# Kernel tuning notes

Measured on AMD Instinct MI355X. Metric: run time of the kernel, lower is better.

## Reference

```python
import jax, jax.numpy as jnp
import numpy as np

LS = 64                      # latent_scaling
TYPES = [8, 1, 1]            # Pyr, SST, VIP widths
DEPTHS = [1, 1, 1]           # L4, L23, L5
B, T = 64, 256
I = 2 * 1 * len(TYPES) * len(DEPTHS)          # 18
AREA = sum(TYPES) * sum(DEPTHS) * LS          # 1920 per area
H = 2 * AREA                                  # 3840


def _build_mask():
    """Block-structured Bernoulli sign mask over 2 areas x (3 layers x 3 types).

    Mirrors the BB* buffers of celltypeRNN: within-area blocks drawn
    Bernoulli(p) with sign +1 for Pyr sources, -1 for SST/VIP sources;
    cross-area blocks zero.
    """
    rng = np.random.default_rng(0)
    # population order per area: (L4,Pyr),(L4,SST),(L4,VIP),(L23,...),(L5,...)
    sizes = [DEPTHS[l] * TYPES[t] * LS for l in range(3) for t in range(3)]
    offs = np.concatenate([[0], np.cumsum(sizes)])
    n_pop = 9
    # connection probability table P[src, dst] (from the source's pvals;
    # unspecified pairs default to 0.05)
    P = np.full((n_pop, n_pop), 0.05)
    # self blocks (diagonal): L4 [.1,.01,.03], L23 [.06,.05,.01], L5 [.04,.03,.03]
    diag = [0.10, 0.01, 0.03, 0.06, 0.05, 0.01, 0.04, 0.03, 0.03]
    for i, p in enumerate(diag):
        P[i, i] = p
    # L4Pyr (idx 0) -> others
    for dst, p in [(1, .04), (4, .04), (7, .03), (2, .00), (5, .02), (8, .11), (3, .07), (6, .00)]:
        P[0, dst] = p
    # L4SST (idx 1) -> others
    for dst, p in [(0, .22), (3, .33), (6, .08), (2, .22), (5, .21), (8, .07), (4, .05), (7, .04)]:
        P[1, dst] = p
    # L4VIP (idx 2) -> Pyr
    P[2, 0] = 0.0
    P[2, 3] = 0.0
    sign = np.array([+1.0, -1.0, -1.0] * 3)  # Pyr +, SST -, VIP -
    mask = np.zeros((H, H), dtype=np.float32)
    for area in range(2):           # V1, LM (within-area connectivity only)
        base = area * AREA
        for s in range(n_pop):
            for d in range(n_pop):
                r0, r1 = base + offs[d], base + offs[d + 1]
                c0, c1 = base + offs[s], base + offs[s + 1]
                blk = (rng.random((r1 - r0, c1 - c0)) < P[s, d]).astype(np.float32)
                mask[r0:r1, c0:c1] = blk * sign[s]
    return jnp.asarray(mask)


def setup_inputs() -> dict:
    key = jax.random.key(0)
    kx, kwi, kbi, kwh, kbh = jax.random.split(key, 5)
    s = 1.0 / np.sqrt(H)
    return {
        "x": jax.random.normal(kx, (B, T, I), jnp.float32),
        "W_ih": jax.random.uniform(kwi, (H, I), jnp.float32, -s, s),
        "b_ih": jax.random.uniform(kbi, (H,), jnp.float32, -s, s),
        "W_hh": jax.random.uniform(kwh, (H, H), jnp.float32, -s, s),
        "b_hh": jax.random.uniform(kbh, (H,), jnp.float32, -s, s),
        "mask": _build_mask(),
    }


def reference(x, W_ih, b_ih, W_hh, b_hh, mask):
    # cell-type connectivity mask applied to the recurrent weights
    Wm = W_hh * mask                              # [H, H]
    # precompute input projection for all timesteps: [B, T, H]
    xp = jnp.einsum("bti,hi->bth", x, W_ih) + b_ih + b_hh
    h0 = jnp.zeros((x.shape[0], Wm.shape[0]), x.dtype)

    def step(h, xp_t):                            # h: [B, H], xp_t: [B, H]
        h = jax.nn.relu(xp_t + h @ Wm.T)
        return h, h

    _, hs = jax.lax.scan(step, h0, jnp.swapaxes(xp, 0, 1))  # [T, B, H]
    return jnp.swapaxes(hs, 0, 1)                            # [B, T, H]
```

## Files before the change

### kernel.cpp

```cpp
#include <hip/hip_runtime.h>
#include <stdint.h>
#include <stddef.h>

#define HH 3840
#define AH 1920
#define NI 18
#define NT 256
#define NBATCH 64
#define KMAX 224
#define JSLOT 28
#define NRW 120
#define NB 8
#define NGROUP 16
#define NBLK_G 16
#define NBLOCKS 256
#define NTHREADS 1024
#define COLS 1920
#define COLT 1938
#define HNEW_PAD 9

#define ENT_BYTES ((size_t)HH * KMAX * 4)
#define CNT_BYTES ((size_t)HH * 4)
#define XT2_BYTES ((size_t)NT * NI * NBATCH * 2)
#define HT_HALF   ((size_t)NGROUP * AH * NB)
#define HT_BYTES  (2 * HT_HALF * 2)
#define FLAG_ELEMS ((size_t)NGROUP * NBLK_G * 32)
#define PC_ELEMS  16
#define PERM_BYTES ((size_t)HH * 4)

#define SLAB_B    (COLT * 16)
#define OFF_HNEW  (2 * SLAB_B)
#define HNEW_B    (2 * NRW * HNEW_PAD * 4)
#define OFF_IPERM (OFF_HNEW + HNEW_B)
#define SMEM_USED (OFF_IPERM + NRW * 4)
#define SMEM_ALLOC 83968

#define AS1 __attribute__((address_space(1)))
#define AS3 __attribute__((address_space(3)))

typedef unsigned long long u64;

__device__ __forceinline__ float lo16(uint32_t u) {
    union { uint16_t q; _Float16 h; } c; c.q = (uint16_t)u; return (float)c.h;
}
__device__ __forceinline__ uint16_t f2h_bits(float f) {
    union { _Float16 h; uint16_t u; } c; c.h = (_Float16)f; return c.u;
}
__device__ __forceinline__ uint32_t pkrtz(float x, float y) {
    typedef __fp16 h2 __attribute__((ext_vector_type(2)));
    union { h2 h; uint32_t u; } c; c.h = __builtin_amdgcn_cvt_pkrtz(x, y); return c.u;
}
__device__ __forceinline__ void gll16(const void* g, void* l) {
    __builtin_amdgcn_global_load_lds((const AS1 uint32_t*)g, (AS3 uint32_t*)l, 16, 0, 0);
}
__device__ __forceinline__ void astore(u64* p, u64 v) {
    __hip_atomic_store(p, v, __ATOMIC_RELAXED, __HIP_MEMORY_SCOPE_AGENT);
}
__device__ __forceinline__ uint32_t sel8(const uint32_t v[8], int b) {
    uint32_t x = v[0];
    #pragma unroll
    for (int i = 1; i < 8; ++i) x = (b == i) ? v[i] : x;
    return x;
}
__device__ __forceinline__ u64 sel8_64(const u64 v[8], int b) {
    u64 x = v[0];
    #pragma unroll
    for (int i = 1; i < 8; ++i) x = (b == i) ? v[i] : x;
    return x;
}
#define SWZ(v, pat) __uint_as_float(__builtin_amdgcn_ds_swizzle(__float_as_uint(v), pat))
#define DPA(c, ctrl) c += __uint_as_float(__builtin_amdgcn_mov_dpp(__float_as_uint(c), ctrl, 0xF, 0xF, true))
#define FMIX_LO(acc, h2, w) asm("v_fma_mix_f32 %0, %1, %2, %0 op_sel:[0,0,0] op_sel_hi:[1,0,0]" : "+v"(acc) : "v"(h2), "v"(w))
#define FMIX_HI(acc, h2, w) asm("v_fma_mix_f32 %0, %1, %2, %0 op_sel:[1,0,0] op_sel_hi:[1,0,0]" : "+v"(acc) : "v"(h2), "v"(w))

__global__ void init_ws_kernel(uint32_t* __restrict__ flg, uint32_t* __restrict__ ht0) {
    size_t i = (size_t)blockIdx.x * blockDim.x + threadIdx.x;
    if (i < FLAG_ELEMS + PC_ELEMS) flg[i] = 0;
    if (i < HT_HALF / 2) ht0[i] = 0;
}

__global__ void deg_kernel(const float* __restrict__ mask, uint32_t* __restrict__ deg) {
    int gw = (int)((blockIdx.x * blockDim.x + threadIdx.x) >> 6);
    int lane = threadIdx.x & 63;
    if (gw >= HH) return;
    int area = (gw >= AH) ? 1 : 0;
    const float* mrow = mask + (size_t)gw * HH + (size_t)area * AH;
    uint32_t n = 0;
    for (int c0 = 0; c0 < AH; c0 += 64)
        n += (uint32_t)__popcll(__ballot(mrow[c0 + lane] != 0.0f));
    if (lane == 0) deg[gw] = n + NI;
}

__global__ void perm_kernel(const uint32_t* __restrict__ deg,
                            uint32_t* __restrict__ posA, uint32_t* __restrict__ invA) {
    int d = blockIdx.x * blockDim.x + threadIdx.x;
    if (d >= HH) return;
    int area = (d >= AH) ? 1 : 0;
    int i = d - area * AH;
    const uint32_t* db = deg + (size_t)area * AH;
    uint32_t di = db[i];
    uint32_t rank = 0;
    for (int j = 0; j < AH; ++j) {
        uint32_t dj = db[j];
        rank += (dj > di || (dj == di && j < i)) ? 1u : 0u;
    }
    uint32_t chunk = rank >> 3, o = rank & 7;
    uint32_t pos = (chunk & 15) * NRW + (chunk >> 4) * 8 + o;
    posA[d] = pos;
    invA[(size_t)area * AH + pos] = (uint32_t)i;
}

__global__ void build_ell_kernel(const float* __restrict__ Whh, const float* __restrict__ mask,
                                 const float* __restrict__ Wih,
                                 const uint32_t* __restrict__ posA, const uint32_t* __restrict__ invA,
                                 uint32_t* __restrict__ ent, uint32_t* __restrict__ cnt) {
    int gw = (int)((blockIdx.x * blockDim.x + threadIdx.x) >> 6);
    int lane = threadIdx.x & 63;
    if (gw >= HH) return;
    const int area = (gw >= AH) ? 1 : 0;
    const int ol = (int)invA[gw];
    const size_t og = (size_t)area * AH + ol;
    const float* mrow = mask + og * HH + (size_t)area * AH;
    const float* wrow = Whh + og * HH + (size_t)area * AH;
    const uint32_t* pA = posA + (size_t)area * AH;
    uint32_t* erow = ent + (size_t)gw * KMAX;
    const u64 below = ((u64)1 << lane) - 1;

    uint32_t sz[8] = {0, 0, 0, 0, 0, 0, 0, 0};
    for (int c0 = 0; c0 <= AH; c0 += 64) {
        bool isx = (c0 == AH);
        bool pred; int b;
        if (isx) { pred = (lane < NI); b = lane & 7; }
        else     { pred = (mrow[c0 + lane] != 0.0f); b = (int)(pA[c0 + lane] & 7); }
        #pragma unroll
        for (int bb = 0; bb < 8; ++bb)
            sz[bb] += (uint32_t)__popcll(__ballot(pred && (b == bb)));
    }
    uint32_t run[8] = {0, 0, 0, 0, 0, 0, 0, 0};
    for (int c0 = 0; c0 <= AH; c0 += 64) {
        bool isx = (c0 == AH);
        int col; bool pred; float wval; int b;
        if (isx) {
            col = COLS + lane; pred = (lane < NI); b = lane & 7;
            wval = pred ? Wih[og * NI + lane] : 0.0f;
        } else {
            float m = mrow[c0 + lane];
            pred = (m != 0.0f);
            col = (int)pA[c0 + lane];
            b = col & 7;
            wval = pred ? wrow[c0 + lane] * m : 0.0f;
        }
        u64 bal[8];
        #pragma unroll
        for (int bb = 0; bb < 8; ++bb) bal[bb] = __ballot(pred && (b == bb));
        if (pred) {
            uint32_t k = sel8(run, b) + (uint32_t)__popcll(sel8_64(bal, b) & below);
            uint32_t rank = k;
            #pragma unroll
            for (int bb = 0; bb < 8; ++bb) {
                uint32_t cap = (bb < b) ? (k + 1) : k;
                uint32_t add = (sz[bb] < cap) ? sz[bb] : cap;
                rank += (bb == b) ? 0u : add;
            }
            if (rank < KMAX) erow[rank] = ((uint32_t)col << 16) | (uint32_t)f2h_bits(wval);
        }
        #pragma unroll
        for (int bb = 0; bb < 8; ++bb) run[bb] += (uint32_t)__popcll(bal[bb]);
    }
    uint32_t tot = sz[0] + sz[1] + sz[2] + sz[3] + sz[4] + sz[5] + sz[6] + sz[7];
    if (lane == 0) cnt[gw] = (tot < KMAX) ? tot : KMAX;
}

__global__ void xt_kernel(const float* __restrict__ x, uint16_t* __restrict__ xT2) {
    int i = blockIdx.x * blockDim.x + threadIdx.x;
    if (i >= NT * NI * NBATCH) return;
    int b = i % NBATCH;
    int rest = i / NBATCH;
    int ii = rest % NI;
    int t = rest / NI;
    xT2[i] = f2h_bits(x[((size_t)b * NT + t) * NI + ii]);
}

__global__ __launch_bounds__(NTHREADS, 4) void rnn_kernel(
    const uint32_t* __restrict__ ent, const uint32_t* __restrict__ cnt,
    const uint16_t* __restrict__ xT2, uint16_t* __restrict__ hT,
    uint32_t* __restrict__ flg, const uint32_t* __restrict__ invA,
    const float* __restrict__ bih, const float* __restrict__ bhh,
    float* __restrict__ out)
{
    extern __shared__ char smem[];
    uint4* slab = (uint4*)smem;
    float* hnew = (float*)(smem + OFF_HNEW);
    uint32_t* iperm = (uint32_t*)(smem + OFF_IPERM);

    const int tid = threadIdx.x;
    const int G = blockIdx.x & 15, role = blockIdx.x >> 4;
    const int a = G >> 3, g = G & 7;
    const int row0 = role * NRW;
    const size_t mySlot = ((size_t)G * NBLK_G + role) * 32;

    const int wv = tid >> 6, lane = tid & 63;
    const int ro = lane >> 3;
    const int kq = lane & 7;
    const int r  = wv * 8 + ro;

    for (int i = tid; i < NRW; i += NTHREADS)
        iperm[i] = invA[(size_t)a * AH + row0 + i];

    float wj[JSLOT];
    int   aj[JSLOT];
    float biasr = 0.f;
    int wm = 0;
    if (wv < 15) {
        const int gRow = a * AH + row0 + r;
        const int ol = (int)invA[gRow];
        const int n = (int)cnt[gRow];
        biasr = bih[a * AH + ol] + bhh[a * AH + ol];
        int jmax = (n > kq) ? ((n - kq + 7) >> 3) : 0;
        const uint32_t* ep = ent + (size_t)gRow * KMAX;
        #pragma unroll
        for (int j = 0; j < JSLOT; ++j) {
            uint32_t e = (j < jmax) ? ep[kq + 8 * j] : 0u;
            aj[j] = (int)((e >> 16) * 16);
            wj[j] = (j < jmax) ? lo16(e) : 0.0f;
        }
        wm = jmax;
        #pragma unroll
        for (int s = 1; s < 64; s <<= 1) {
            int ov = __shfl_xor(wm, s, 64);
            wm = (ov > wm) ? ov : wm;
        }
    }

    for (int t = 0; t < NT; ++t) {
        const int cur = t & 1, nxt = cur ^ 1;
        if (wv == 0 && lane < NI)
            gll16(xT2 + ((size_t)t * NI + lane) * NBATCH + g * NB,
                  &slab[cur * COLT + COLS + lane]);
        if (wv > 0 || t == 0) {
            const int p = (role + wv) & 15;
            if (t > 0) {
                const uint32_t* sl = flg + ((size_t)G * NBLK_G + p) * 32;
                int guard = 0;
                while (__hip_atomic_load(sl, __ATOMIC_RELAXED, __HIP_MEMORY_SCOPE_AGENT)
                       < (uint32_t)t && ++guard < (1 << 15))
                    __builtin_amdgcn_s_sleep(1);
            }
            const uint4* sp = (const uint4*)(hT + (size_t)cur * HT_HALF
                                             + ((size_t)G * AH + p * NRW) * NB);
            const int l2 = (lane < 56) ? (64 + lane) : lane;
            uint4 v0, v1;
            asm volatile("global_load_dwordx4 %0, %2, off sc0 sc1\n\t"
                         "global_load_dwordx4 %1, %3, off sc0 sc1\n\t"
                         "s_waitcnt vmcnt(0)"
                         : "=&v"(v0), "=&v"(v1)
                         : "v"(sp + lane), "v"(sp + l2)
                         : "memory");
            uint4* dst = slab + cur * COLT + p * NRW;
            dst[lane] = v0;
            dst[l2] = v1;
        }
        __syncthreads();

        if (wv == 15 && t > 0) {
            const float* hp = hnew + ((t - 1) & 1) * NRW * HNEW_PAD;
            for (int i = lane; i < NB * NRW; i += 64) {
                int bb = i / NRW, d = i - bb * NRW;
                out[(((size_t)(g * NB + bb)) * NT + (t - 1)) * HH + (size_t)a * AH + iperm[d]]
                    = hp[d * HNEW_PAD + bb];
            }
        }

        if (wv < 15) {
            const char* sb = (const char*)(slab + cur * COLT);
            float c0 = 0.f, c1 = 0.f, c2 = 0.f, c3 = 0.f, c4 = 0.f, c5 = 0.f, c6 = 0.f, c7 = 0.f;
            #pragma unroll
            for (int j = 0; j < JSLOT; ++j) {
                if (j >= wm) break;
                const uint4 hv = *(const uint4*)(sb + aj[j]);
                const float wf = wj[j];
                FMIX_LO(c0, hv.x, wf); FMIX_HI(c1, hv.x, wf);
                FMIX_LO(c2, hv.y, wf); FMIX_HI(c3, hv.y, wf);
                FMIX_LO(c4, hv.z, wf); FMIX_HI(c5, hv.z, wf);
                FMIX_LO(c6, hv.w, wf); FMIX_HI(c7, hv.w, wf);
            }
            c0 += SWZ(c0, 0x101F); c1 += SWZ(c1, 0x101F); c2 += SWZ(c2, 0x101F); c3 += SWZ(c3, 0x101F);
            c4 += SWZ(c4, 0x101F); c5 += SWZ(c5, 0x101F); c6 += SWZ(c6, 0x101F); c7 += SWZ(c7, 0x101F);
            DPA(c0, 0x4E); DPA(c1, 0x4E); DPA(c2, 0x4E); DPA(c3, 0x4E);
            DPA(c4, 0x4E); DPA(c5, 0x4E); DPA(c6, 0x4E); DPA(c7, 0x4E);
            DPA(c0, 0xB1); DPA(c1, 0xB1); DPA(c2, 0xB1); DPA(c3, 0xB1);
            DPA(c4, 0xB1); DPA(c5, 0xB1); DPA(c6, 0xB1); DPA(c7, 0xB1);
            if (kq == 0) {
                float h0 = fmaxf(c0 + biasr, 0.f), h1 = fmaxf(c1 + biasr, 0.f);
                float h2 = fmaxf(c2 + biasr, 0.f), h3 = fmaxf(c3 + biasr, 0.f);
                float h4 = fmaxf(c4 + biasr, 0.f), h5 = fmaxf(c5 + biasr, 0.f);
                float h6 = fmaxf(c6 + biasr, 0.f), h7 = fmaxf(c7 + biasr, 0.f);
                uint4 pk;
                pk.x = pkrtz(h0, h1); pk.y = pkrtz(h2, h3);
                pk.z = pkrtz(h4, h5); pk.w = pkrtz(h6, h7);
                u64* dst8 = (u64*)(hT + (size_t)nxt * HT_HALF
                                   + ((size_t)G * AH + row0 + r) * NB);
                astore(dst8,     ((u64)pk.y << 32) | pk.x);
                astore(dst8 + 1, ((u64)pk.w << 32) | pk.z);
                slab[nxt * COLT + row0 + r] = pk;
                float* hp = hnew + cur * NRW * HNEW_PAD + r * HNEW_PAD;
                hp[0] = h0; hp[1] = h1; hp[2] = h2; hp[3] = h3;
                hp[4] = h4; hp[5] = h5; hp[6] = h6; hp[7] = h7;
            }
        }
        __syncthreads();

        if (tid == 0)
            __hip_atomic_store(flg + mySlot, (uint32_t)(t + 1), __ATOMIC_RELAXED,
                               __HIP_MEMORY_SCOPE_AGENT);
    }
    {
        const float* hp = hnew + ((NT - 1) & 1) * NRW * HNEW_PAD;
        for (int i = tid; i < NB * NRW; i += NTHREADS) {
            int bb = i / NRW, d = i - bb * NRW;
            out[(((size_t)(g * NB + bb)) * NT + (NT - 1)) * HH + (size_t)a * AH + iperm[d]]
                = hp[d * HNEW_PAD + bb];
        }
    }
}

extern "C" void kernel_launch(void* const* d_in, const int* in_sizes, int n_in,
                              void* d_out, int out_size, void* d_ws, size_t ws_size,
                              hipStream_t stream)
{
    const float* x    = (const float*)d_in[0];
    const float* Wih  = (const float*)d_in[1];
    const float* bih  = (const float*)d_in[2];
    const float* Whh  = (const float*)d_in[3];
    const float* bhh  = (const float*)d_in[4];
    const float* mask = (const float*)d_in[5];
    float* out = (float*)d_out;

    char* ws = (char*)d_ws;
    uint32_t* ent = (uint32_t*)(ws);
    uint32_t* cnt = (uint32_t*)(ws + ENT_BYTES);
    uint16_t* xT2 = (uint16_t*)(ws + ENT_BYTES + CNT_BYTES);
    uint16_t* hT  = (uint16_t*)(ws + ENT_BYTES + CNT_BYTES + XT2_BYTES);
    uint32_t* flg = (uint32_t*)(ws + ENT_BYTES + CNT_BYTES + XT2_BYTES + HT_BYTES);
    char* ptail   = ws + ENT_BYTES + CNT_BYTES + XT2_BYTES + HT_BYTES
                    + (FLAG_ELEMS + PC_ELEMS) * 4;
    uint32_t* posA = (uint32_t*)(ptail);
    uint32_t* invA = (uint32_t*)(ptail + PERM_BYTES);
    uint32_t* degA = (uint32_t*)(ptail + 2 * PERM_BYTES);

    init_ws_kernel<<<512, 256, 0, stream>>>(flg, (uint32_t*)hT);
    deg_kernel<<<(HH * 64 + 255) / 256, 256, 0, stream>>>(mask, degA);
    perm_kernel<<<(HH + 255) / 256, 256, 0, stream>>>(degA, posA, invA);
    build_ell_kernel<<<(HH * 64 + 255) / 256, 256, 0, stream>>>(Whh, mask, Wih, posA, invA, ent, cnt);
    xt_kernel<<<(NT * NI * NBATCH + 255) / 256, 256, 0, stream>>>(x, xT2);

    hipFuncSetAttribute((const void*)rnn_kernel,
                        hipFuncAttributeMaxDynamicSharedMemorySize, SMEM_ALLOC);

    void* args[] = {(void*)&ent, (void*)&cnt, (void*)&xT2, (void*)&hT, (void*)&flg,
                    (void*)&invA, (void*)&bih, (void*)&bhh, (void*)&out};
    hipLaunchCooperativeKernel((const void*)rnn_kernel, dim3(NBLOCKS), dim3(NTHREADS),
                               args, SMEM_ALLOC, stream);
}
```

Measured before the change: 1.136 ms.

## Split batch into 32 groups of 4 to double cooperative block count

Each batch group now holds 4 sequences instead of 8, so there are 32 groups and 512 cooperative blocks, two per CU rather than one. The aim is more parallel work per timestep and shorter per-block gather/FMA chains, with the LDS slab halved to 8 bytes per column and the x loads switched to 4-byte global_load_lds. The cost is twice as many inter-block flags and h exchanges per step, each sparse weight entry read twice as often across blocks, and higher register pressure from launch bounds of 8.

Result: slower. 3.093 ms (+172.3%).

```diff
diff --git a/kernel.cpp b/kernel.cpp
--- a/kernel.cpp
+++ b/kernel.cpp
@@ -10,14 +10,14 @@
 #define KMAX 224
 #define JSLOT 28
 #define NRW 120
-#define NB 8
-#define NGROUP 16
+#define NB 4
+#define NGROUP 32
 #define NBLK_G 16
-#define NBLOCKS 256
+#define NBLOCKS 512
 #define NTHREADS 1024
 #define COLS 1920
 #define COLT 1938
-#define HNEW_PAD 9
+#define HNEW_PAD 5
 
 #define ENT_BYTES ((size_t)HH * KMAX * 4)
 #define CNT_BYTES ((size_t)HH * 4)
@@ -28,12 +28,11 @@
 #define PC_ELEMS  16
 #define PERM_BYTES ((size_t)HH * 4)
 
-#define SLAB_B    (COLT * 16)
+#define SLAB_B    (COLT * 8)
 #define OFF_HNEW  (2 * SLAB_B)
 #define HNEW_B    (2 * NRW * HNEW_PAD * 4)
 #define OFF_IPERM (OFF_HNEW + HNEW_B)
-#define SMEM_USED (OFF_IPERM + NRW * 4)
-#define SMEM_ALLOC 83968
+#define SMEM_ALLOC (OFF_IPERM + NRW * 4)
 
 #define AS1 __attribute__((address_space(1)))
 #define AS3 __attribute__((address_space(3)))
@@ -50,8 +49,8 @@
     typedef __fp16 h2 __attribute__((ext_vector_type(2)));
     union { h2 h; uint32_t u; } c; c.h = __builtin_amdgcn_cvt_pkrtz(x, y); return c.u;
 }
-__device__ __forceinline__ void gll16(const void* g, void* l) {
-    __builtin_amdgcn_global_load_lds((const AS1 uint32_t*)g, (AS3 uint32_t*)l, 16, 0, 0);
+__device__ __forceinline__ void gll4(const void* g, void* l) {
+    __builtin_amdgcn_global_load_lds((const AS1 uint32_t*)g, (AS3 uint32_t*)l, 4, 0, 0);
 }
 __device__ __forceinline__ void astore(u64* p, u64 v) {
     __hip_atomic_store(p, v, __ATOMIC_RELAXED, __HIP_MEMORY_SCOPE_AGENT);
@@ -181,7 +180,7 @@
     xT2[i] = f2h_bits(x[((size_t)b * NT + t) * NI + ii]);
 }
 
-__global__ __launch_bounds__(NTHREADS, 4) void rnn_kernel(
+__global__ __launch_bounds__(NTHREADS, 8) void rnn_kernel(
     const uint32_t* __restrict__ ent, const uint32_t* __restrict__ cnt,
     const uint16_t* __restrict__ xT2, uint16_t* __restrict__ hT,
     uint32_t* __restrict__ flg, const uint32_t* __restrict__ invA,
@@ -189,13 +188,12 @@
     float* __restrict__ out)
 {
     extern __shared__ char smem[];
-    uint4* slab = (uint4*)smem;
     float* hnew = (float*)(smem + OFF_HNEW);
     uint32_t* iperm = (uint32_t*)(smem + OFF_IPERM);
 
     const int tid = threadIdx.x;
-    const int G = blockIdx.x & 15, role = blockIdx.x >> 4;
-    const int a = G >> 3, g = G & 7;
+    const int G = (blockIdx.x >> 4) & 31, role = blockIdx.x & 15;
+    const int a = G >> 4, btile = G & 15;
     const int row0 = role * NRW;
     const size_t mySlot = ((size_t)G * NBLK_G + role) * 32;
 
@@ -221,7 +219,7 @@
         #pragma unroll
         for (int j = 0; j < JSLOT; ++j) {
             uint32_t e = (j < jmax) ? ep[kq + 8 * j] : 0u;
-            aj[j] = (int)((e >> 16) * 16);
+            aj[j] = (int)((e >> 16) * 8);
             wj[j] = (j < jmax) ? lo16(e) : 0.0f;
         }
         wm = jmax;
@@ -234,9 +232,12 @@
 
     for (int t = 0; t < NT; ++t) {
         const int cur = t & 1, nxt = cur ^ 1;
-        if (wv == 0 && lane < NI)
-            gll16(xT2 + ((size_t)t * NI + lane) * NBATCH + g * NB,
-                  &slab[cur * COLT + COLS + lane]);
+        char* sbc = smem + cur * SLAB_B;
+        if (wv == 0 && lane < 2 * NI) {
+            const uint16_t* xs = xT2 + ((size_t)t * NI + (lane >> 1)) * NBATCH
+                                 + btile * NB + (lane & 1) * 2;
+            gll4(xs, (uint32_t*)(sbc + COLS * 8) + lane);
+        }
         if (wv > 0 || t == 0) {
             const int p = (role + wv) & 15;
             if (t > 0) {
@@ -246,19 +247,15 @@
                        < (uint32_t)t && ++guard < (1 << 15))
                     __builtin_amdgcn_s_sleep(1);
             }
-            const uint4* sp = (const uint4*)(hT + (size_t)cur * HT_HALF
-                                             + ((size_t)G * AH + p * NRW) * NB);
-            const int l2 = (lane < 56) ? (64 + lane) : lane;
-            uint4 v0, v1;
-            asm volatile("global_load_dwordx4 %0, %2, off sc0 sc1\n\t"
-                         "global_load_dwordx4 %1, %3, off sc0 sc1\n\t"
-                         "s_waitcnt vmcnt(0)"
-                         : "=&v"(v0), "=&v"(v1)
-                         : "v"(sp + lane), "v"(sp + l2)
-                         : "memory");
-            uint4* dst = slab + cur * COLT + p * NRW;
-            dst[lane] = v0;
-            dst[l2] = v1;
+            if (lane < 60) {
+                const uint4* sp = (const uint4*)(hT + (size_t)cur * HT_HALF
+                                                 + ((size_t)G * AH + p * NRW) * NB);
+                uint4 v0;
+                asm volatile("global_load_dwordx4 %0, %1, off sc0 sc1\n\t"
+                             "s_waitcnt vmcnt(0)"
+                             : "=&v"(v0) : "v"(sp + lane) : "memory");
+                ((uint4*)(sbc + p * NRW * 8))[lane] = v0;
+            }
         }
         __syncthreads();
 
@@ -266,46 +263,35 @@
             const float* hp = hnew + ((t - 1) & 1) * NRW * HNEW_PAD;
             for (int i = lane; i < NB * NRW; i += 64) {
                 int bb = i / NRW, d = i - bb * NRW;
-                out[(((size_t)(g * NB + bb)) * NT + (t - 1)) * HH + (size_t)a * AH + iperm[d]]
+                out[(((size_t)(btile * NB + bb)) * NT + (t - 1)) * HH + (size_t)a * AH + iperm[d]]
                     = hp[d * HNEW_PAD + bb];
             }
         }
 
         if (wv < 15) {
-            const char* sb = (const char*)(slab + cur * COLT);
-            float c0 = 0.f, c1 = 0.f, c2 = 0.f, c3 = 0.f, c4 = 0.f, c5 = 0.f, c6 = 0.f, c7 = 0.f;
+            float c0 = 0.f, c1 = 0.f, c2 = 0.f, c3 = 0.f;
             #pragma unroll
             for (int j = 0; j < JSLOT; ++j) {
                 if (j >= wm) break;
-                const uint4 hv = *(const uint4*)(sb + aj[j]);
+                const uint2 hv = *(const uint2*)(sbc + aj[j]);
                 const float wf = wj[j];
                 FMIX_LO(c0, hv.x, wf); FMIX_HI(c1, hv.x, wf);
                 FMIX_LO(c2, hv.y, wf); FMIX_HI(c3, hv.y, wf);
-                FMIX_LO(c4, hv.z, wf); FMIX_HI(c5, hv.z, wf);
-                FMIX_LO(c6, hv.w, wf); FMIX_HI(c7, hv.w, wf);
-            }
-            c0 += SWZ(c0, 0x101F); c1 += SWZ(c1, 0x101F); c2 += SWZ(c2, 0x101F); c3 += SWZ(c3, 0x101F);
-            c4 += SWZ(c4, 0x101F); c5 += SWZ(c5, 0x101F); c6 += SWZ(c6, 0x101F); c7 += SWZ(c7, 0x101F);
+            }
+            c0 += SWZ(c0, 0x101F); c1 += SWZ(c1, 0x101F);
+            c2 += SWZ(c2, 0x101F); c3 += SWZ(c3, 0x101F);
             DPA(c0, 0x4E); DPA(c1, 0x4E); DPA(c2, 0x4E); DPA(c3, 0x4E);
-            DPA(c4, 0x4E); DPA(c5, 0x4E); DPA(c6, 0x4E); DPA(c7, 0x4E);
             DPA(c0, 0xB1); DPA(c1, 0xB1); DPA(c2, 0xB1); DPA(c3, 0xB1);
-            DPA(c4, 0xB1); DPA(c5, 0xB1); DPA(c6, 0xB1); DPA(c7, 0xB1);
             if (kq == 0) {
                 float h0 = fmaxf(c0 + biasr, 0.f), h1 = fmaxf(c1 + biasr, 0.f);
                 float h2 = fmaxf(c2 + biasr, 0.f), h3 = fmaxf(c3 + biasr, 0.f);
-                float h4 = fmaxf(c4 + biasr, 0.f), h5 = fmaxf(c5 + biasr, 0.f);
-                float h6 = fmaxf(c6 + biasr, 0.f), h7 = fmaxf(c7 + biasr, 0.f);
-                uint4 pk;
-                pk.x = pkrtz(h0, h1); pk.y = pkrtz(h2, h3);
-                pk.z = pkrtz(h4, h5); pk.w = pkrtz(h6, h7);
+                uint32_t p0 = pkrtz(h0, h1), p1 = pkrtz(h2, h3);
                 u64* dst8 = (u64*)(hT + (size_t)nxt * HT_HALF
                                    + ((size_t)G * AH + row0 + r) * NB);
-                astore(dst8,     ((u64)pk.y << 32) | pk.x);
-                astore(dst8 + 1, ((u64)pk.w << 32) | pk.z);
-                slab[nxt * COLT + row0 + r] = pk;
+                astore(dst8, ((u64)p1 << 32) | p0);
+                *(uint2*)(smem + nxt * SLAB_B + (row0 + r) * 8) = make_uint2(p0, p1);
                 float* hp = hnew + cur * NRW * HNEW_PAD + r * HNEW_PAD;
                 hp[0] = h0; hp[1] = h1; hp[2] = h2; hp[3] = h3;
-                hp[4] = h4; hp[5] = h5; hp[6] = h6; hp[7] = h7;
             }
         }
         __syncthreads();
@@ -318,7 +304,7 @@
         const float* hp = hnew + ((NT - 1) & 1) * NRW * HNEW_PAD;
         for (int i = tid; i < NB * NRW; i += NTHREADS) {
             int bb = i / NRW, d = i - bb * NRW;
-            out[(((size_t)(g * NB + bb)) * NT + (NT - 1)) * HH + (size_t)a * AH + iperm[d]]
+            out[(((size_t)(btile * NB + bb)) * NT + (NT - 1)) * HH + (size_t)a * AH + iperm[d]]
                 = hp[d * HNEW_PAD + bb];
         }
     }
@@ -348,7 +334,7 @@
     uint32_t* invA = (uint32_t*)(ptail + PERM_BYTES);
     uint32_t* degA = (uint32_t*)(ptail + 2 * PERM_BYTES);
 
-    init_ws_kernel<<<512, 256, 0, stream>>>(flg, (uint32_t*)hT);
+    init_ws_kernel<<<1024, 256, 0, stream>>>(flg, (uint32_t*)hT);
     deg_kernel<<<(HH * 64 + 255) / 256, 256, 0, stream>>>(mask, degA);
     perm_kernel<<<(HH + 255) / 256, 256, 0, stream>>>(degA, posA, invA);
     build_ell_kernel<<<(HH * 64 + 255) / 256, 256, 0, stream>>>(Whh, mask, Wih, posA, invA, ent, cnt);
```
